# Optimization experiments

Hardware: AMD Instinct MI355X
Metric: run time of the kernel (lower is better)

The kernel has to match this reference:

```python
import jax, jax.numpy as jnp
import numpy as np

B, T, C, HD = 4, 4096, 1024, 64  # batch, seq, n_embd, head_dim = n_embd//n_head


def setup_inputs() -> dict:
    key = jax.random.key(0)
    k1, k2, k3, k4 = jax.random.split(key, 4)
    scale = 0.02
    return {
        "x": jax.random.normal(k1, (B, T, C), dtype=jnp.float32),
        "Wq": jax.random.normal(k2, (C, HD), dtype=jnp.float32) * scale,
        "Wk": jax.random.normal(k3, (C, HD), dtype=jnp.float32) * scale,
        "Wv": jax.random.normal(k4, (C, HD), dtype=jnp.float32) * scale,
    }


def reference(x, Wq, Wk, Wv):
    # single-head projections: [B,T,C] @ [C,HD] -> [B,T,HD]
    q = jnp.einsum("btc,ch->bth", x, Wq)
    k = jnp.einsum("btc,ch->bth", x, Wk)
    v = jnp.einsum("btc,ch->bth", x, Wv)
    scale = k.shape[-1] ** -0.5
    # scores: [B,T,T], causal mask via -inf, stable softmax
    alpha = jnp.einsum("bqh,bkh->bqk", q, k) * scale
    t = x.shape[1]
    causal = jnp.tril(jnp.ones((t, t), dtype=bool))
    alpha = jnp.where(causal, alpha, -jnp.inf)
    alpha = jax.nn.softmax(alpha, axis=-1)
    # dropout p=0.0 -> identity
    h = jnp.einsum("bqk,bkh->bqh", alpha, v)
    return h
```

## Files before the change

### kernel.cpp

```cpp
#include <hip/hip_runtime.h>

#define T_SEQ 4096
#define C_DIM 1024
#define HD 64
#define NCH 272

typedef __attribute__((ext_vector_type(8))) __bf16 bf16x8;
typedef __attribute__((ext_vector_type(8))) unsigned short us8;
typedef __attribute__((ext_vector_type(4))) unsigned short us4;
typedef __attribute__((ext_vector_type(4))) float f32x4;
typedef __attribute__((ext_vector_type(16))) float f32x16;

#define QSCALE 0.18033688011112042f

__device__ __forceinline__ unsigned short f2bf(float f) {
    union { float f; unsigned u; } x; x.f = f;
    unsigned r = x.u + 0x7FFFu + ((x.u >> 16) & 1u);
    return (unsigned short)(r >> 16);
}

__device__ __forceinline__ float bf2f(unsigned short u) {
    union { unsigned u; float f; } x; x.u = ((unsigned)u) << 16;
    return x.f;
}

__device__ __forceinline__ us8 cvt8(float4 a, float4 b) {
    union { __bf16 h[8]; us8 v; } u;
    u.h[0] = (__bf16)a.x; u.h[1] = (__bf16)a.y; u.h[2] = (__bf16)a.z; u.h[3] = (__bf16)a.w;
    u.h[4] = (__bf16)b.x; u.h[5] = (__bf16)b.y; u.h[6] = (__bf16)b.z; u.h[7] = (__bf16)b.w;
    return u.v;
}

__device__ __forceinline__ us4 cvt4f(float a, float b, float c, float d) {
    union { __bf16 h[4]; us4 v; } u;
    u.h[0] = (__bf16)a; u.h[1] = (__bf16)b; u.h[2] = (__bf16)c; u.h[3] = (__bf16)d;
    return u.v;
}

__device__ __forceinline__ f32x16 zero16() {
    f32x16 v;
    #pragma unroll
    for (int j = 0; j < 16; ++j) v[j] = 0.f;
    return v;
}

__device__ __forceinline__ int swzs(int idx) {
    return idx ^ ((((idx) >> 6) & 7) << 3);
}

__device__ __forceinline__ int offf(int qt) {
    const int m = qt >> 1;
    return (qt & 1) ? (m + 1) * (m + 1) : m * m + m;
}

__global__ __launch_bounds__(256) void k_wtrans(const float* __restrict__ Wq,
                                                const float* __restrict__ Wk,
                                                const float* __restrict__ Wv,
                                                unsigned short* __restrict__ wt_g) {
    __shared__ unsigned short tile[64][72];
    const int bx = blockIdx.x;
    const int which = bx >> 4;
    const int k0 = (bx & 15) * 64;
    const float* W = (which == 0) ? Wq : ((which == 1) ? Wk : Wv);
    const int t = threadIdx.x;
    {
        const int r = t >> 2, c0 = (t & 3) * 16;
        const float4* src = reinterpret_cast<const float4*>(W + (k0 + r) * HD + c0);
        #pragma unroll
        for (int i = 0; i < 4; ++i) {
            float4 v = src[i];
            tile[r][c0 + 4 * i + 0] = f2bf(v.x);
            tile[r][c0 + 4 * i + 1] = f2bf(v.y);
            tile[r][c0 + 4 * i + 2] = f2bf(v.z);
            tile[r][c0 + 4 * i + 3] = f2bf(v.w);
        }
    }
    __syncthreads();
    {
        const int n = t >> 2, kc0 = (t & 3) * 16;
        alignas(16) unsigned short o[16];
        #pragma unroll
        for (int i = 0; i < 16; ++i) o[i] = tile[kc0 + i][n];
        unsigned short* dst = wt_g + (size_t)(which * 64 + n) * 1024 + k0 + kc0;
        *reinterpret_cast<us8*>(dst)     = *reinterpret_cast<const us8*>(&o[0]);
        *reinterpret_cast<us8*>(dst + 8) = *reinterpret_cast<const us8*>(&o[8]);
    }
}

__global__ __launch_bounds__(512) void k_proj(const float* __restrict__ x,
                                              const unsigned short* __restrict__ wt_g,
                                              unsigned short* __restrict__ qs,
                                              unsigned short* __restrict__ ksb,
                                              unsigned short* __restrict__ vt) {
    __shared__ unsigned short smem[13312];
    unsigned short* xs0 = smem;
    unsigned short* xs1 = smem + 4608;
    const int tid = threadIdx.x;
    const int w = tid >> 6, lane = tid & 63;
    const int l15 = lane & 15, g = lane >> 4;
    const int wm = w & 1, wn = w >> 1;
    const int m0 = blockIdx.x * 64;
    const int sr = tid >> 3, sc0 = (tid & 7) * 8;
    const float* xrow = x + (size_t)(m0 + sr) * C_DIM + sc0;
    const unsigned short* wrow[3];
    #pragma unroll
    for (int mf = 0; mf < 3; ++mf)
        wrow[mf] = wt_g + (size_t)((3 * wn + mf) * 16 + l15) * C_DIM + g * 8;

    f32x4 acc[3][2];
    #pragma unroll
    for (int mf = 0; mf < 3; ++mf)
        #pragma unroll
        for (int nf = 0; nf < 2; ++nf)
            acc[mf][nf] = (f32x4){0.f, 0.f, 0.f, 0.f};

    {
        float4 xa = *reinterpret_cast<const float4*>(xrow);
        float4 xb = *reinterpret_cast<const float4*>(xrow + 4);
        *reinterpret_cast<us8*>(xs0 + sr * 72 + sc0) = cvt8(xa, xb);
    }
    us8 wc[3][2];
    #pragma unroll
    for (int mf = 0; mf < 3; ++mf)
        #pragma unroll
        for (int k2 = 0; k2 < 2; ++k2)
            wc[mf][k2] = *reinterpret_cast<const us8*>(wrow[mf] + k2 * 32);
    __syncthreads();

    for (int kk = 0; kk < 16; ++kk) {
        unsigned short* xcur = (kk & 1) ? xs1 : xs0;
        unsigned short* xnxt = (kk & 1) ? xs0 : xs1;
        const bool pf = (kk < 15);
        float4 na, nb;
        us8 wn2[3][2];
        if (pf) {
            na = *reinterpret_cast<const float4*>(xrow + (kk + 1) * 64);
            nb = *reinterpret_cast<const float4*>(xrow + (kk + 1) * 64 + 4);
            #pragma unroll
            for (int mf = 0; mf < 3; ++mf)
                #pragma unroll
                for (int k2 = 0; k2 < 2; ++k2)
                    wn2[mf][k2] = *reinterpret_cast<const us8*>(wrow[mf] + (kk + 1) * 64 + k2 * 32);
        }
        #pragma unroll
        for (int k2 = 0; k2 < 2; ++k2) {
            bf16x8 bfr[2];
            #pragma unroll
            for (int nf = 0; nf < 2; ++nf)
                bfr[nf] = *reinterpret_cast<const bf16x8*>(
                    xcur + (wm * 32 + nf * 16 + l15) * 72 + k2 * 32 + g * 8);
            #pragma unroll
            for (int mf = 0; mf < 3; ++mf) {
                bf16x8 afr = *reinterpret_cast<const bf16x8*>(&wc[mf][k2]);
                #pragma unroll
                for (int nf = 0; nf < 2; ++nf)
                    acc[mf][nf] = __builtin_amdgcn_mfma_f32_16x16x32_bf16(
                        afr, bfr[nf], acc[mf][nf], 0, 0, 0);
            }
        }
        if (pf) {
            *reinterpret_cast<us8*>(xnxt + sr * 72 + sc0) = cvt8(na, nb);
            #pragma unroll
            for (int mf = 0; mf < 3; ++mf)
                #pragma unroll
                for (int k2 = 0; k2 < 2; ++k2)
                    wc[mf][k2] = wn2[mf][k2];
        }
        __syncthreads();
    }

    unsigned short* out_lds = smem;
    #pragma unroll
    for (int mf = 0; mf < 3; ++mf) {
        const int Mfr = 3 * wn + mf;
        const float s = (Mfr < 4) ? QSCALE : 1.0f;
        #pragma unroll
        for (int nf = 0; nf < 2; ++nf) {
            union { __bf16 h[4]; us4 v; } u;
            #pragma unroll
            for (int r = 0; r < 4; ++r) u.h[r] = (__bf16)(acc[mf][nf][r] * s);
            *reinterpret_cast<us4*>(
                out_lds + (wm * 32 + nf * 16 + l15) * 208 + Mfr * 16 + 4 * g) = u.v;
        }
    }
    __syncthreads();
    {
        const int r = tid >> 3, c = (tid & 7) * 8;
        const size_t gm = (size_t)(m0 + r);
        *reinterpret_cast<us8*>(qs + gm * 64 + c)  = *reinterpret_cast<const us8*>(out_lds + r * 208 + c);
        *reinterpret_cast<us8*>(ksb + gm * 64 + c) = *reinterpret_cast<const us8*>(out_lds + r * 208 + 64 + c);
    }
    {
        const int d = tid >> 3, j0 = (tid & 7) * 8;
        const int b = m0 >> 12, t0 = m0 & 4095;
        alignas(16) unsigned short tmp[8];
        #pragma unroll
        for (int j = 0; j < 8; ++j) tmp[j] = out_lds[(j0 + j) * 208 + 128 + d];
        *reinterpret_cast<us8*>(vt + (size_t)(b * 64 + d) * T_SEQ + t0 + j0) =
            *reinterpret_cast<const us8*>(tmp);
    }
}

__global__ __launch_bounds__(256) void k_attn(const unsigned short* __restrict__ qs,
                                              const unsigned short* __restrict__ ks,
                                              const unsigned short* __restrict__ vt,
                                              unsigned short* __restrict__ Opart,
                                              float* __restrict__ lw,
                                              float* __restrict__ out) {
    __shared__ unsigned short sm[16384];
    const int tid = threadIdx.x;
    const int w = tid >> 6, lane = tid & 63;
    const int l31 = lane & 31, hi = lane >> 5;
    const int batch = blockIdx.y;
    const int i = (NCH - 1) - blockIdx.x;
    int qt = min(31, (int)(2.0f * sqrtf((float)i)));
    while (offf(qt + 1) <= i) ++qt;
    while (offf(qt) > i) --qt;
    const int s = i - offf(qt);
    const int ns = (qt + 2) >> 1;
    const int it0 = s * 4;
    const int it1 = min(it0 + 4, 2 * qt + 2);
    const int qi = qt * 128 + 32 * w + l31;
    const size_t qrow = (size_t)batch * T_SEQ + qi;

    bf16x8 qf[4];
    #pragma unroll
    for (int df = 0; df < 4; ++df)
        qf[df] = *reinterpret_cast<const bf16x8*>(qs + qrow * 64 + df * 16 + hi * 8);

    f32x16 accO0 = zero16(), accO1 = zero16();
    float lp0 = 0.f, lp1 = 0.f, lp2 = 0.f, lp3 = 0.f;

    const int sr = tid >> 2, sc0 = (tid & 3) * 16;
    const unsigned short* kbase = ks + ((size_t)batch * T_SEQ + sr) * 64 + sc0;
    const unsigned short* vbase = vt + ((size_t)batch * 64 + sr) * T_SEQ + sc0;

    {
        us8 a0 = *reinterpret_cast<const us8*>(kbase + (size_t)it0 * 4096);
        us8 a1 = *reinterpret_cast<const us8*>(kbase + (size_t)it0 * 4096 + 8);
        us8 b0 = *reinterpret_cast<const us8*>(vbase + it0 * 64);
        us8 b1 = *reinterpret_cast<const us8*>(vbase + it0 * 64 + 8);
        us8 w0, w1;
        #pragma unroll
        for (int j = 0; j < 4; ++j) { w0[j] = b0[j]; w0[4 + j] = b1[j]; w1[j] = b0[4 + j]; w1[4 + j] = b1[4 + j]; }
        const int kd = sr * 64 + sc0, vd = 8192 + sr * 64 + sc0;
        *reinterpret_cast<us8*>(sm + swzs(kd))     = a0;
        *reinterpret_cast<us8*>(sm + swzs(kd + 8)) = a1;
        *reinterpret_cast<us8*>(sm + swzs(vd))     = w0;
        *reinterpret_cast<us8*>(sm + swzs(vd + 8)) = w1;
    }
    __syncthreads();

    for (int it = it0; it < it1; ++it) {
        const int cur = (it - it0) & 1;
        const bool pf = (it + 1 < it1);
        us8 n0, n1, m0, m1;
        if (pf) {
            n0 = *reinterpret_cast<const us8*>(kbase + (size_t)(it + 1) * 4096);
            n1 = *reinterpret_cast<const us8*>(kbase + (size_t)(it + 1) * 4096 + 8);
            m0 = *reinterpret_cast<const us8*>(vbase + (it + 1) * 64);
            m1 = *reinterpret_cast<const us8*>(vbase + (it + 1) * 64 + 8);
        }
        const int kb = cur * 4096;
        const int vb = 8192 + cur * 4096;
        const bool diag = (it >= 2 * qt);

        #pragma unroll
        for (int ksub = 0; ksub < 2; ++ksub) {
            f32x16 sv = zero16();
            __builtin_amdgcn_s_setprio(1);
            #pragma unroll
            for (int df = 0; df < 4; ++df) {
                bf16x8 afr = *reinterpret_cast<const bf16x8*>(
                    sm + swzs(kb + (ksub * 32 + l31) * 64 + df * 16 + hi * 8));
                sv = __builtin_amdgcn_mfma_f32_32x32x16_bf16(afr, qf[df], sv, 0, 0, 0);
            }
            __builtin_amdgcn_s_setprio(0);
            if (diag) {
                #pragma unroll
                for (int rr = 0; rr < 16; ++rr) {
                    const int kidx = it * 64 + ksub * 32 + (rr & 3) + 8 * (rr >> 2) + 4 * hi;
                    if (kidx > qi) sv[rr] = -1e30f;
                }
            }
            f32x16 pv;
            #pragma unroll
            for (int rr = 0; rr < 16; ++rr) pv[rr] = exp2f(sv[rr]);
            #pragma unroll
            for (int rr = 0; rr < 4; ++rr) {
                lp0 += pv[4 * rr + 0];
                lp1 += pv[4 * rr + 1];
                lp2 += pv[4 * rr + 2];
                lp3 += pv[4 * rr + 3];
            }
            us8 bfr0, bfr1;
            {
                us4 c0 = cvt4f(pv[0], pv[1], pv[2], pv[3]);
                us4 c1 = cvt4f(pv[4], pv[5], pv[6], pv[7]);
                us4 c2 = cvt4f(pv[8], pv[9], pv[10], pv[11]);
                us4 c3 = cvt4f(pv[12], pv[13], pv[14], pv[15]);
                #pragma unroll
                for (int j = 0; j < 4; ++j) {
                    bfr0[j] = c0[j]; bfr0[4 + j] = c1[j];
                    bfr1[j] = c2[j]; bfr1[4 + j] = c3[j];
                }
            }
            __builtin_amdgcn_s_setprio(1);
            {
                bf16x8 a00 = *reinterpret_cast<const bf16x8*>(
                    sm + swzs(vb + l31 * 64 + ksub * 32 + hi * 8));
                bf16x8 a01 = *reinterpret_cast<const bf16x8*>(
                    sm + swzs(vb + l31 * 64 + ksub * 32 + 16 + hi * 8));
                accO0 = __builtin_amdgcn_mfma_f32_32x32x16_bf16(
                    a00, *reinterpret_cast<bf16x8*>(&bfr0), accO0, 0, 0, 0);
                accO0 = __builtin_amdgcn_mfma_f32_32x32x16_bf16(
                    a01, *reinterpret_cast<bf16x8*>(&bfr1), accO0, 0, 0, 0);
                bf16x8 a10 = *reinterpret_cast<const bf16x8*>(
                    sm + swzs(vb + (32 + l31) * 64 + ksub * 32 + hi * 8));
                bf16x8 a11 = *reinterpret_cast<const bf16x8*>(
                    sm + swzs(vb + (32 + l31) * 64 + ksub * 32 + 16 + hi * 8));
                accO1 = __builtin_amdgcn_mfma_f32_32x32x16_bf16(
                    a10, *reinterpret_cast<bf16x8*>(&bfr0), accO1, 0, 0, 0);
                accO1 = __builtin_amdgcn_mfma_f32_32x32x16_bf16(
                    a11, *reinterpret_cast<bf16x8*>(&bfr1), accO1, 0, 0, 0);
            }
            __builtin_amdgcn_s_setprio(0);
        }
        if (pf) {
            us8 w0, w1;
            #pragma unroll
            for (int j = 0; j < 4; ++j) { w0[j] = m0[j]; w0[4 + j] = m1[j]; w1[j] = m0[4 + j]; w1[4 + j] = m1[4 + j]; }
            const int kd = (cur ^ 1) * 4096 + sr * 64 + sc0;
            const int vd = 8192 + (cur ^ 1) * 4096 + sr * 64 + sc0;
            *reinterpret_cast<us8*>(sm + swzs(kd))     = n0;
            *reinterpret_cast<us8*>(sm + swzs(kd + 8)) = n1;
            *reinterpret_cast<us8*>(sm + swzs(vd))     = w0;
            *reinterpret_cast<us8*>(sm + swzs(vd + 8)) = w1;
        }
        __syncthreads();
    }

    float l_run = (lp0 + lp1) + (lp2 + lp3);
    l_run += __shfl_xor(l_run, 32, 64);

    if (ns == 1) {
        const float inv = 1.0f / l_run;
        #pragma unroll
        for (int rg = 0; rg < 4; ++rg) {
            const int d0 = 4 * hi + 8 * rg;
            f32x4 o0 = {accO0[4 * rg] * inv, accO0[4 * rg + 1] * inv,
                        accO0[4 * rg + 2] * inv, accO0[4 * rg + 3] * inv};
            f32x4 o1 = {accO1[4 * rg] * inv, accO1[4 * rg + 1] * inv,
                        accO1[4 * rg + 2] * inv, accO1[4 * rg + 3] * inv};
            *reinterpret_cast<f32x4*>(out + qrow * 64 + d0)      = o0;
            *reinterpret_cast<f32x4*>(out + qrow * 64 + 32 + d0) = o1;
        }
    } else {
        const int pb = batch * NCH + i;
        const int q = 32 * w + l31;
        unsigned short* ob = Opart + (size_t)pb * 8192 + q * 64;
        #pragma unroll
        for (int rg = 0; rg < 4; ++rg) {
            const int d0 = 4 * hi + 8 * rg;
            *reinterpret_cast<us4*>(ob + d0) =
                cvt4f(accO0[4 * rg], accO0[4 * rg + 1], accO0[4 * rg + 2], accO0[4 * rg + 3]);
            *reinterpret_cast<us4*>(ob + 32 + d0) =
                cvt4f(accO1[4 * rg], accO1[4 * rg + 1], accO1[4 * rg + 2], accO1[4 * rg + 3]);
        }
        if (hi == 0) lw[(size_t)pb * 128 + q] = l_run;
    }
}

__global__ __launch_bounds__(256) void k_combine(const unsigned short* __restrict__ Opart,
                                                 const float* __restrict__ lw,
                                                 float* __restrict__ out) {
    const int qt = 2 + (blockIdx.x >> 1), half = blockIdx.x & 1;
    const int batch = blockIdx.y;
    const int t = threadIdx.x;
    const int q = half * 64 + (t >> 2), d0 = (t & 3) * 16;
    const int ns = (qt + 2) >> 1;
    const int pb0 = batch * NCH + offf(qt);
    float num[16];
    #pragma unroll
    for (int j = 0; j < 16; ++j) num[j] = 0.f;
    float lsum = 0.f;
    for (int s = 0; s < ns; ++s) {
        const int pb = pb0 + s;
        lsum += lw[(size_t)pb * 128 + q];
        const unsigned short* op = Opart + (size_t)pb * 8192 + q * 64 + d0;
        us8 v0 = *reinterpret_cast<const us8*>(op);
        us8 v1 = *reinterpret_cast<const us8*>(op + 8);
        #pragma unroll
        for (int j = 0; j < 8; ++j) {
            num[j] += bf2f(v0[j]);
            num[8 + j] += bf2f(v1[j]);
        }
    }
    const float inv = 1.f / lsum;
    float* o = out + ((size_t)batch * T_SEQ + qt * 128 + q) * 64 + d0;
    #pragma unroll
    for (int h = 0; h < 4; ++h) {
        f32x4 v = {num[4 * h] * inv, num[4 * h + 1] * inv,
                   num[4 * h + 2] * inv, num[4 * h + 3] * inv};
        *reinterpret_cast<f32x4*>(o + 4 * h) = v;
    }
}

extern "C" void kernel_launch(void* const* d_in, const int* in_sizes, int n_in,
                              void* d_out, int out_size, void* d_ws, size_t ws_size,
                              hipStream_t stream) {
    (void)in_sizes; (void)n_in; (void)out_size; (void)ws_size;
    const float* x  = (const float*)d_in[0];
    const float* Wq = (const float*)d_in[1];
    const float* Wk = (const float*)d_in[2];
    const float* Wv = (const float*)d_in[3];
    float* out = (float*)d_out;
    unsigned short* ws16 = (unsigned short*)d_ws;
    unsigned short* wt_g  = ws16;
    unsigned short* qsb   = ws16 + 196608;
    unsigned short* ksb   = qsb + 1048576;
    unsigned short* vtb   = ksb + 1048576;
    unsigned short* Opart = vtb + 1048576;
    float* lw = (float*)(Opart + 8912896);
    k_wtrans <<<dim3(48),      dim3(256), 0, stream>>>(Wq, Wk, Wv, wt_g);
    k_proj   <<<dim3(256),     dim3(512), 0, stream>>>(x, wt_g, qsb, ksb, vtb);
    k_attn   <<<dim3(NCH, 4),  dim3(256), 0, stream>>>(qsb, ksb, vtb, Opart, lw, out);
    k_combine<<<dim3(60, 4),   dim3(256), 0, stream>>>(Opart, lw, out);
}
```

Baseline: 71.28 us.

## Stage projection weights through LDS with chunk-major layout and smaller blocks

Reorders the transposed weight buffer so each 64-wide K chunk is contiguous, letting every projection block load the whole weight chunk cooperatively with coalesced 16-byte loads into a double-buffered LDS tile. The projection kernel now uses 256 threads and 32 rows per block (512 blocks), and each wave computes three 16-column output fragments for all rows. This aims to replace scattered per-lane global weight loads and improve occupancy. In exchange it uses more LDS per block and reads the weights once per smaller block.

```diff
diff --git a/kernel.cpp b/kernel.cpp
--- a/kernel.cpp
+++ b/kernel.cpp
@@ -60,7 +60,8 @@
     __shared__ unsigned short tile[64][72];
     const int bx = blockIdx.x;
     const int which = bx >> 4;
-    const int k0 = (bx & 15) * 64;
+    const int kc = bx & 15;
+    const int k0 = kc * 64;
     const float* W = (which == 0) ? Wq : ((which == 1) ? Wk : Wv);
     const int t = threadIdx.x;
     {
@@ -81,31 +82,24 @@
         alignas(16) unsigned short o[16];
         #pragma unroll
         for (int i = 0; i < 16; ++i) o[i] = tile[kc0 + i][n];
-        unsigned short* dst = wt_g + (size_t)(which * 64 + n) * 1024 + k0 + kc0;
+        unsigned short* dst = wt_g + (size_t)kc * 12288 + (which * 64 + n) * 64 + kc0;
         *reinterpret_cast<us8*>(dst)     = *reinterpret_cast<const us8*>(&o[0]);
         *reinterpret_cast<us8*>(dst + 8) = *reinterpret_cast<const us8*>(&o[8]);
     }
 }
 
-__global__ __launch_bounds__(512) void k_proj(const float* __restrict__ x,
+__global__ __launch_bounds__(256) void k_proj(const float* __restrict__ x,
                                               const unsigned short* __restrict__ wt_g,
                                               unsigned short* __restrict__ qs,
                                               unsigned short* __restrict__ ksb,
                                               unsigned short* __restrict__ vt) {
-    __shared__ unsigned short smem[13312];
-    unsigned short* xs0 = smem;
-    unsigned short* xs1 = smem + 4608;
+    __shared__ unsigned short smem[32256];
     const int tid = threadIdx.x;
     const int w = tid >> 6, lane = tid & 63;
     const int l15 = lane & 15, g = lane >> 4;
-    const int wm = w & 1, wn = w >> 1;
-    const int m0 = blockIdx.x * 64;
+    const int m0 = blockIdx.x * 32;
     const int sr = tid >> 3, sc0 = (tid & 7) * 8;
     const float* xrow = x + (size_t)(m0 + sr) * C_DIM + sc0;
-    const unsigned short* wrow[3];
-    #pragma unroll
-    for (int mf = 0; mf < 3; ++mf)
-        wrow[mf] = wt_g + (size_t)((3 * wn + mf) * 16 + l15) * C_DIM + g * 8;
 
     f32x4 acc[3][2];
     #pragma unroll
@@ -117,30 +111,32 @@
     {
         float4 xa = *reinterpret_cast<const float4*>(xrow);
         float4 xb = *reinterpret_cast<const float4*>(xrow + 4);
-        *reinterpret_cast<us8*>(xs0 + sr * 72 + sc0) = cvt8(xa, xb);
-    }
-    us8 wc[3][2];
-    #pragma unroll
-    for (int mf = 0; mf < 3; ++mf)
-        #pragma unroll
-        for (int k2 = 0; k2 < 2; ++k2)
-            wc[mf][k2] = *reinterpret_cast<const us8*>(wrow[mf] + k2 * 32);
+        *reinterpret_cast<us8*>(smem + sr * 72 + sc0) = cvt8(xa, xb);
+        #pragma unroll
+        for (int j = 0; j < 6; ++j) {
+            const int li = tid + 256 * j;
+            us8 v = *reinterpret_cast<const us8*>(wt_g + li * 8);
+            *reinterpret_cast<us8*>(smem + 4608 + (li >> 3) * 72 + (li & 7) * 8) = v;
+        }
+    }
     __syncthreads();
 
     for (int kk = 0; kk < 16; ++kk) {
-        unsigned short* xcur = (kk & 1) ? xs1 : xs0;
-        unsigned short* xnxt = (kk & 1) ? xs0 : xs1;
+        const int cur = kk & 1;
         const bool pf = (kk < 15);
+        const int xb = cur * 2304;
+        const int wb = 4608 + cur * 13824;
+        const int xbn = (cur ^ 1) * 2304;
+        const int wbn = 4608 + (cur ^ 1) * 13824;
         float4 na, nb;
-        us8 wn2[3][2];
+        us8 wn[6];
         if (pf) {
             na = *reinterpret_cast<const float4*>(xrow + (kk + 1) * 64);
             nb = *reinterpret_cast<const float4*>(xrow + (kk + 1) * 64 + 4);
-            #pragma unroll
-            for (int mf = 0; mf < 3; ++mf)
-                #pragma unroll
-                for (int k2 = 0; k2 < 2; ++k2)
-                    wn2[mf][k2] = *reinterpret_cast<const us8*>(wrow[mf] + (kk + 1) * 64 + k2 * 32);
+            const unsigned short* wsrc = wt_g + (size_t)(kk + 1) * 12288;
+            #pragma unroll
+            for (int j = 0; j < 6; ++j)
+                wn[j] = *reinterpret_cast<const us8*>(wsrc + (tid + 256 * j) * 8);
         }
         #pragma unroll
         for (int k2 = 0; k2 < 2; ++k2) {
@@ -148,10 +144,11 @@
             #pragma unroll
             for (int nf = 0; nf < 2; ++nf)
                 bfr[nf] = *reinterpret_cast<const bf16x8*>(
-                    xcur + (wm * 32 + nf * 16 + l15) * 72 + k2 * 32 + g * 8);
+                    smem + xb + (nf * 16 + l15) * 72 + k2 * 32 + g * 8);
             #pragma unroll
             for (int mf = 0; mf < 3; ++mf) {
-                bf16x8 afr = *reinterpret_cast<const bf16x8*>(&wc[mf][k2]);
+                bf16x8 afr = *reinterpret_cast<const bf16x8*>(
+                    smem + wb + ((3 * w + mf) * 16 + l15) * 72 + k2 * 32 + g * 8);
                 #pragma unroll
                 for (int nf = 0; nf < 2; ++nf)
                     acc[mf][nf] = __builtin_amdgcn_mfma_f32_16x16x32_bf16(
@@ -159,12 +156,12 @@
             }
         }
         if (pf) {
-            *reinterpret_cast<us8*>(xnxt + sr * 72 + sc0) = cvt8(na, nb);
-            #pragma unroll
-            for (int mf = 0; mf < 3; ++mf)
-                #pragma unroll
-                for (int k2 = 0; k2 < 2; ++k2)
-                    wc[mf][k2] = wn2[mf][k2];
+            *reinterpret_cast<us8*>(smem + xbn + sr * 72 + sc0) = cvt8(na, nb);
+            #pragma unroll
+            for (int j = 0; j < 6; ++j) {
+                const int li = tid + 256 * j;
+                *reinterpret_cast<us8*>(smem + wbn + (li >> 3) * 72 + (li & 7) * 8) = wn[j];
+            }
         }
         __syncthreads();
     }
@@ -172,15 +169,14 @@
     unsigned short* out_lds = smem;
     #pragma unroll
     for (int mf = 0; mf < 3; ++mf) {
-        const int Mfr = 3 * wn + mf;
+        const int Mfr = 3 * w + mf;
         const float s = (Mfr < 4) ? QSCALE : 1.0f;
         #pragma unroll
         for (int nf = 0; nf < 2; ++nf) {
             union { __bf16 h[4]; us4 v; } u;
             #pragma unroll
             for (int r = 0; r < 4; ++r) u.h[r] = (__bf16)(acc[mf][nf][r] * s);
-            *reinterpret_cast<us4*>(
-                out_lds + (wm * 32 + nf * 16 + l15) * 208 + Mfr * 16 + 4 * g) = u.v;
+            *reinterpret_cast<us4*>(out_lds + (nf * 16 + l15) * 208 + Mfr * 16 + 4 * g) = u.v;
         }
     }
     __syncthreads();
@@ -191,7 +187,7 @@
         *reinterpret_cast<us8*>(ksb + gm * 64 + c) = *reinterpret_cast<const us8*>(out_lds + r * 208 + 64 + c);
     }
     {
-        const int d = tid >> 3, j0 = (tid & 7) * 8;
+        const int d = tid >> 2, j0 = (tid & 3) * 8;
         const int b = m0 >> 12, t0 = m0 & 4095;
         alignas(16) unsigned short tmp[8];
         #pragma unroll
@@ -423,7 +419,7 @@
     unsigned short* Opart = vtb + 1048576;
     float* lw = (float*)(Opart + 8912896);
     k_wtrans <<<dim3(48),      dim3(256), 0, stream>>>(Wq, Wk, Wv, wt_g);
-    k_proj   <<<dim3(256),     dim3(512), 0, stream>>>(x, wt_g, qsb, ksb, vtb);
+    k_proj   <<<dim3(512),     dim3(256), 0, stream>>>(x, wt_g, qsb, ksb, vtb);
     k_attn   <<<dim3(NCH, 4),  dim3(256), 0, stream>>>(qsb, ksb, vtb, Opart, lw, out);
     k_combine<<<dim3(60, 4),   dim3(256), 0, stream>>>(Opart, lw, out);
 }
```

Measured after the change: 61.08 us (median of 2 runs). 14.3% less time.
